# Kernel tuning notes

Hardware: AMD Instinct MI355X
Metric: run time of the kernel (lower is better)

## Reference

```python
import jax, jax.numpy as jnp
import numpy as np

ADMP = 8  # admp_channel -> K = ADMP*ADMP keypoints


def setup_inputs() -> dict:
    key = jax.random.key(0)
    kA, kB = jax.random.split(key)
    B, C, H, W = 8, 512, 96, 96
    feature_A = jax.random.normal(kA, (B, C, H, W), dtype=jnp.float32)
    feature_B = jax.random.normal(kB, (B, C, H, W), dtype=jnp.float32)
    return {"feature_A": feature_A, "feature_B": feature_B}


def _keypoint_rowcol(feature_A):
    # featureSelect: sum over channels, AdaptiveMaxPool2d(ADMP) with return_indices.
    # H,W divisible by ADMP so adaptive pool == uniform non-overlapping pooling.
    B, C, H, W = feature_A.shape
    ph, pw = H // ADMP, W // ADMP
    resp = feature_A.sum(axis=1)  # [B,H,W]
    r = resp.reshape(B, ADMP, ph, ADMP, pw).transpose(0, 1, 3, 2, 4)
    r = r.reshape(B, ADMP * ADMP, ph * pw)
    loc = jnp.argmax(r, axis=-1)  # first-max, matches torch  [B,K]
    kk = jnp.arange(ADMP * ADMP)
    gi, gj = kk // ADMP, kk % ADMP
    row_A = gi[None, :] * ph + loc // pw  # [B,K]
    col_A = gj[None, :] * pw + loc % pw
    return row_A, col_A


def reference(feature_A, feature_B):
    B, C, H, W = feature_A.shape
    K = ADMP * ADMP
    row_A, col_A = _keypoint_rowcol(feature_A)
    flat_A = row_A * W + col_A  # [B,K]

    # gather descriptors: [B,K,C]
    fa = feature_A.reshape(B, C, H * W)
    desc = jnp.take_along_axis(fa, flat_A[:, None, :], axis=2).transpose(0, 2, 1)

    # squared L2 distance map via ||b||^2 - 2 a.b + ||a||^2 : [B,K,HW]
    fb = feature_B.reshape(B, C, H * W)
    fb_sq = jnp.sum(fb * fb, axis=1)            # [B,HW]
    d_sq = jnp.sum(desc * desc, axis=-1)        # [B,K]
    cross = jnp.einsum('bkc,bcn->bkn', desc, fb)  # [B,K,HW]
    dist = fb_sq[:, None, :] - 2.0 * cross + d_sq[:, :, None]

    min_idx = jnp.argmin(dist, axis=-1)  # [B,K]
    row_B = min_idx // W
    col_B = min_idx % W
    drow = -(row_B - row_A)
    dcol = -(col_B - col_A)
    off = jnp.stack([drow, dcol], axis=-1)  # [B,K,2] int

    # getTranslationalOffsetByMode: most frequent (drow,dcol) pair per batch
    eq = jnp.all(off[:, :, None, :] == off[:, None, :, :], axis=-1)  # [B,K,K]
    counts = eq.sum(axis=-1)  # [B,K]
    best = jnp.argmax(counts, axis=-1)  # first occurrence on ties, matches dict order
    out = jnp.take_along_axis(off, best[:, None, None], axis=1)[:, 0, :]  # [B,2]
    return out
```

## Files before the change

### kernel.cpp

```cpp
#include <hip/hip_runtime.h>
#include <hip/hip_bf16.h>
#include <math.h>

typedef _Float16 half8 __attribute__((ext_vector_type(8)));
typedef __fp16 fp16x2 __attribute__((ext_vector_type(2)));
typedef float f32x4 __attribute__((ext_vector_type(4)));
typedef unsigned short u16x4 __attribute__((ext_vector_type(4)));
typedef unsigned short u16x8 __attribute__((ext_vector_type(8)));
typedef unsigned long long u64;

#define B_   8
#define C_   512
#define H_   96
#define W_   96
#define HW   9216
#define K_   64
#define PH   12
#define PW   12
#define NT   96
#define CCH  32
#define NBLK 96

#define OFF_PARTIAL 0u
#define OFF_DESCH   2359296u
#define OFF_DESCL   2883584u
#define OFF_ROWA    3407872u
#define OFF_COLA    3409920u
#define OFF_SLOTS   3411968u

#define FBT_HI 0
#define FBT_LO 3072
#define DSC_HI 6144
#define DSC_LO 8704
#define BUFHW  11264

__global__ __launch_bounds__(256) void k_partial(const float* __restrict__ A,
                                                 float* __restrict__ part,
                                                 u64* __restrict__ slots) {
    if (blockIdx.x == 0 && blockIdx.y == 0) {
        slots[threadIdx.x] = ~0ull;
        slots[threadIdx.x + 256] = ~0ull;
    }
    int bxs = (blockIdx.x & 7) * 9 + (blockIdx.x >> 3);
    int idx4 = bxs * 256 + threadIdx.x;
    int chunk = blockIdx.y;
    int b = idx4 / (HW / 4), hw4 = idx4 - b * (HW / 4);
    const float* p = A + ((size_t)(b * C_ + chunk * 64)) * HW + hw4 * 4;
    float4 s = make_float4(0.f, 0.f, 0.f, 0.f);
#pragma unroll
    for (int i = 0; i < 64; ++i) {
        float4 v = *(const float4*)&p[(size_t)i * HW];
        s.x += v.x; s.y += v.y; s.z += v.z; s.w += v.w;
    }
    *(float4*)&part[chunk * (B_ * HW) + b * HW + hw4 * 4] = s;
}

__global__ void k_selgather(const float* __restrict__ part, const float* __restrict__ A,
                            int* __restrict__ rowA, int* __restrict__ colA,
                            _Float16* __restrict__ descH, _Float16* __restrict__ descL) {
    int k = blockIdx.x, b = blockIdx.y, lane = threadIdx.x;
    int gi = k >> 3, gj = k & 7;
    float bv = -1e30f; int bp = 1 << 20;
    for (int p = lane; p < PH * PW; p += 64) {
        int lr = p / PW, lc = p - lr * PW;
        int hw = (gi * PH + lr) * W_ + gj * PW + lc;
        float v = 0.f;
#pragma unroll
        for (int ch = 0; ch < 8; ++ch) v += part[ch * (B_ * HW) + b * HW + hw];
        if (v > bv || (v == bv && p < bp)) { bv = v; bp = p; }
    }
    for (int m = 1; m < 64; m <<= 1) {
        float ov = __shfl_xor(bv, m);
        int   op = __shfl_xor(bp, m);
        if (ov > bv || (ov == bv && op < bp)) { bv = ov; bp = op; }
    }
    int lr = bp / PW, lc = bp - lr * PW;
    int r = gi * PH + lr, c = gj * PW + lc;
    int flat = r * W_ + c;
    if (lane == 0) { rowA[b * K_ + k] = r; colA[b * K_ + k] = c; }
#pragma unroll
    for (int i = 0; i < 8; ++i) {
        int cc = i * 64 + lane;
        float v = A[((size_t)(b * C_ + cc)) * HW + flat];
        _Float16 h = (_Float16)v;
        _Float16 lo = (_Float16)((v - (float)h) * 2048.f);
        size_t o = ((size_t)(b * K_ + k)) * C_ + cc;
        descH[o] = h; descL[o] = lo;
    }
}

__global__ __launch_bounds__(256, 3) void k_main(const float* __restrict__ FB,
                                                 const _Float16* __restrict__ descH,
                                                 const _Float16* __restrict__ descL,
                                                 u64* __restrict__ slots) {
    __shared__ __attribute__((aligned(16))) unsigned short smem_us[2 * BUFHW];
    int b = blockIdx.y;
    int bxs = (blockIdx.x & 7) * 12 + (blockIdx.x >> 3);
    int nb = bxs * NT;
    int tid = threadIdx.x;
    int l = tid & 63;
    int w = tid >> 6;
    const size_t baseB = (size_t)b * C_ * HW + nb;

    const int so = tid % 12;
    const int scb = tid / 12;
    const int st_nt = so >> 1, st_nn0 = (so & 1) * 8;
    const int dk = tid >> 2, dco = tid & 3;

    f32x4 accH[6], accX[6];
#pragma unroll
    for (int nt = 0; nt < 6; ++nt) {
        accH[nt] = (f32x4){0.f, 0.f, 0.f, 0.f};
        accX[nt] = (f32x4){0.f, 0.f, 0.f, 0.f};
    }
    float sq[8];
#pragma unroll
    for (int j = 0; j < 8; ++j) sq[j] = 0.f;

    float4 Ar0a, Ar0b, Ar1a, Ar1b; u16x8 ArdH, ArdL;
    float4 Br0a, Br0b, Br1a, Br1b; u16x8 BrdH, BrdL;

#define LOADALL(S, c0)                                                        \
    do {                                                                      \
        if (tid < 192) {                                                      \
            const float* p0 = &FB[baseB + (size_t)((c0) + scb) * HW + so * 8];      \
            const float* p1 = &FB[baseB + (size_t)((c0) + scb + 16) * HW + so * 8]; \
            S##r0a = *(const float4*)p0; S##r0b = *(const float4*)(p0 + 4);   \
            S##r1a = *(const float4*)p1; S##r1b = *(const float4*)(p1 + 4);   \
        }                                                                     \
        size_t o = ((size_t)(b * K_) + dk) * C_ + (c0) + dco * 8;             \
        S##rdH = *(const u16x8*)&descH[o];                                    \
        S##rdL = *(const u16x8*)&descL[o];                                    \
    } while (0)

#define CVT8(va, vb, hofs)                                                    \
    do {                                                                      \
        union { fp16x2 p[4]; half8 h; } hh, ll;                               \
        float vv[8] = {va.x, va.y, va.z, va.w, vb.x, vb.y, vb.z, vb.w};       \
        _Pragma("unroll")                                                     \
        for (int j = 0; j < 4; ++j) {                                         \
            float a = vv[2 * j], bq = vv[2 * j + 1];                          \
            fp16x2 hp = __builtin_amdgcn_cvt_pkrtz(a, bq);                    \
            float ha = (float)hp[0], hb = (float)hp[1];                       \
            fp16x2 lp = __builtin_amdgcn_cvt_pkrtz((a - ha) * 2048.f,         \
                                                   (bq - hb) * 2048.f);       \
            hh.p[j] = hp; ll.p[j] = lp;                                       \
            sq[2 * j]     = fmaf(a, a, sq[2 * j]);                            \
            sq[2 * j + 1] = fmaf(bq, bq, sq[2 * j + 1]);                      \
        }                                                                     \
        *(half8*)&smem_us[(hofs)] = hh.h;                                     \
        *(half8*)&smem_us[(hofs) + FBT_LO] = ll.h;                            \
    } while (0)

#define WRITEALL(S, bufhw)                                                    \
    do {                                                                      \
        if (tid < 192) {                                                      \
            int c = scb;                                                      \
            int off0 = (bufhw) + FBT_HI + st_nt * 512 + ((c >> 2) & 1) * 256  \
                       + (c >> 3) * 64 + (c & 3) * 16 + st_nn0;               \
            CVT8(S##r0a, S##r0b, off0);                                       \
            c = scb + 16;                                                     \
            int off1 = (bufhw) + FBT_HI + st_nt * 512 + ((c >> 2) & 1) * 256  \
                       + (c >> 3) * 64 + (c & 3) * 16 + st_nn0;               \
            CVT8(S##r1a, S##r1b, off1);                                       \
        }                                                                     \
        *(u16x8*)&smem_us[(bufhw) + DSC_HI + dk * 40 + dco * 8] = S##rdH;     \
        *(u16x8*)&smem_us[(bufhw) + DSC_LO + dk * 40 + dco * 8] = S##rdL;     \
    } while (0)

    const unsigned lds0 = (unsigned)(size_t)&smem_us[0];

#define TRQ(d0, d1, d2, d3, addr)                                             \
    asm volatile("ds_read_b64_tr_b16 %0, %1"             : "=v"(d0) : "v"(addr)); \
    asm volatile("ds_read_b64_tr_b16 %0, %1 offset:512"  : "=v"(d1) : "v"(addr)); \
    asm volatile("ds_read_b64_tr_b16 %0, %1 offset:6144" : "=v"(d2) : "v"(addr)); \
    asm volatile("ds_read_b64_tr_b16 %0, %1 offset:6656" : "=v"(d3) : "v"(addr));

#define WAIT8 asm volatile("s_waitcnt lgkmcnt(8)" ::: "memory");              \
              __builtin_amdgcn_sched_barrier(0);
#define WAIT4 asm volatile("s_waitcnt lgkmcnt(4)" ::: "memory");              \
              __builtin_amdgcn_sched_barrier(0);
#define WAIT0 asm volatile("s_waitcnt lgkmcnt(0)" ::: "memory");              \
              __builtin_amdgcn_sched_barrier(0);

#define MFMA3(nt, h0_, h1_, l0_, l1_)                                         \
    do {                                                                      \
        union { u16x4 q[2]; half8 h; } bh, bl;                                \
        bh.q[0] = h0_; bh.q[1] = h1_; bl.q[0] = l0_; bl.q[1] = l1_;           \
        accH[nt] = __builtin_amdgcn_mfma_f32_16x16x32_f16(aHu.h, bh.h, accH[nt], 0, 0, 0); \
        accX[nt] = __builtin_amdgcn_mfma_f32_16x16x32_f16(aHu.h, bl.h, accX[nt], 0, 0, 0); \
        accX[nt] = __builtin_amdgcn_mfma_f32_16x16x32_f16(aLu.h, bh.h, accX[nt], 0, 0, 0); \
    } while (0)

#define COMPUTE(cur)                                                          \
    do {                                                                      \
        union { u16x8 u; half8 h; } aHu, aLu;                                 \
        const unsigned abase = lds0 +                                         \
            (unsigned)((cur) + DSC_HI + (w * 16 + (l & 15)) * 40 + (l >> 4) * 8) * 2u; \
        __builtin_amdgcn_s_setprio(1);                                        \
        asm volatile("ds_read_b128 %0, %1"             : "=v"(aHu.u) : "v"(abase)); \
        asm volatile("ds_read_b128 %0, %1 offset:5120" : "=v"(aLu.u) : "v"(abase)); \
        const unsigned trb = lds0 + (unsigned)(cur) * 2u + (unsigned)l * 8u;  \
        u16x4 xh0, xh1, xl0, xl1, yh0, yh1, yl0, yl1, zh0, zh1, zl0, zl1;     \
        TRQ(xh0, xh1, xl0, xl1, trb);                                         \
        TRQ(yh0, yh1, yl0, yl1, trb + 1024u);                                 \
        TRQ(zh0, zh1, zl0, zl1, trb + 2048u);                                 \
        WAIT8;                                                                \
        MFMA3(0, xh0, xh1, xl0, xl1);                                         \
        TRQ(xh0, xh1, xl0, xl1, trb + 3072u);                                 \
        WAIT8;                                                                \
        MFMA3(1, yh0, yh1, yl0, yl1);                                         \
        TRQ(yh0, yh1, yl0, yl1, trb + 4096u);                                 \
        WAIT8;                                                                \
        MFMA3(2, zh0, zh1, zl0, zl1);                                         \
        TRQ(zh0, zh1, zl0, zl1, trb + 5120u);                                 \
        WAIT8;                                                                \
        MFMA3(3, xh0, xh1, xl0, xl1);                                         \
        WAIT4;                                                                \
        MFMA3(4, yh0, yh1, yl0, yl1);                                         \
        WAIT0;                                                                \
        MFMA3(5, zh0, zh1, zl0, zl1);                                         \
        __builtin_amdgcn_s_setprio(0);                                        \
    } while (0)

    LOADALL(A, 0);
    WRITEALL(A, 0);
    LOADALL(B, CCH);
    __syncthreads();

#pragma unroll 1
    for (int tp = 0; tp < 8; ++tp) {
        const int t0 = 2 * tp, t1 = 2 * tp + 1;
        if (t0 + 2 < 16) LOADALL(A, (t0 + 2) * CCH);
        COMPUTE(0);
        if (t0 + 1 < 16) WRITEALL(B, BUFHW);
        __syncthreads();
        if (t1 + 2 < 16) LOADALL(B, (t1 + 2) * CCH);
        COMPUTE(BUFHW);
        if (t1 + 1 < 16) WRITEALL(A, 0);
        __syncthreads();
    }

    float* fscr = (float*)&smem_us[0];
    if (tid < 192) {
        *(float4*)&fscr[scb * 96 + so * 8]     = make_float4(sq[0], sq[1], sq[2], sq[3]);
        *(float4*)&fscr[scb * 96 + so * 8 + 4] = make_float4(sq[4], sq[5], sq[6], sq[7]);
    }
    __syncthreads();
    if (tid < 96) {
        float s = 0.f;
#pragma unroll
        for (int g = 0; g < 16; ++g) s += fscr[g * 96 + tid];
        fscr[1536 + tid] = s;
    }
    __syncthreads();

    const float inv2048 = 1.f / 2048.f;
#pragma unroll
    for (int r = 0; r < 4; ++r) {
        float bv = 1e30f; int bn = 1 << 28;
#pragma unroll
        for (int nt = 0; nt < 6; ++nt) {
            float cross = accH[nt][r] + accX[nt][r] * inv2048;
            float d = fscr[1536 + nt * 16 + (l & 15)] - 2.f * cross;
            int n = nb + nt * 16 + (l & 15);
            if (d < bv) { bv = d; bn = n; }
        }
#pragma unroll
        for (int m = 1; m < 16; m <<= 1) {
            float ov = __shfl_xor(bv, m);
            int   on = __shfl_xor(bn, m);
            if (ov < bv || (ov == bv && on < bn)) { bv = ov; bn = on; }
        }
        if ((l & 15) == 0) {
            int k = w * 16 + (l >> 4) * 4 + r;
            unsigned bits = __float_as_uint(bv);
            unsigned key = (bits & 0x80000000u) ? ~bits : (bits | 0x80000000u);
            u64 packed = ((u64)key << 32) | (unsigned)bn;
            atomicMin(&slots[b * K_ + k], packed);
        }
    }
#undef LOADALL
#undef CVT8
#undef WRITEALL
#undef TRQ
#undef WAIT8
#undef WAIT4
#undef WAIT0
#undef MFMA3
#undef COMPUTE
}

__global__ void k_redmode(const u64* __restrict__ slots,
                          const int* __restrict__ rowA, const int* __restrict__ colA,
                          int* __restrict__ out) {
    __shared__ int r_s[64], c_s[64];
    int b = blockIdx.x, k = threadIdx.x;
    u64 s = slots[b * K_ + k];
    int bn = (int)(unsigned)(s & 0xFFFFFFFFull);
    int rB = bn / W_, cB = bn - rB * W_;
    r_s[k] = rowA[b * K_ + k] - rB;
    c_s[k] = colA[b * K_ + k] - cB;
    __syncthreads();
    int mr = r_s[k], mc = c_s[k], cnt = 0;
#pragma unroll
    for (int j = 0; j < 64; ++j) cnt += (r_s[j] == mr && c_s[j] == mc) ? 1 : 0;
    int bk = k, bc = cnt;
    for (int m = 1; m < 64; m <<= 1) {
        int oc = __shfl_xor(bc, m);
        int ok = __shfl_xor(bk, m);
        if (oc > bc || (oc == bc && ok < bk)) { bc = oc; bk = ok; }
    }
    if (k == 0) { out[b * 2] = r_s[bk]; out[b * 2 + 1] = c_s[bk]; }
}

extern "C" void kernel_launch(void* const* d_in, const int* in_sizes, int n_in,
                              void* d_out, int out_size, void* d_ws, size_t ws_size,
                              hipStream_t stream) {
    const float* A  = (const float*)d_in[0];
    const float* FB = (const float*)d_in[1];
    char* ws = (char*)d_ws;
    float*     part  = (float*)(ws + OFF_PARTIAL);
    _Float16*  descH = (_Float16*)(ws + OFF_DESCH);
    _Float16*  descL = (_Float16*)(ws + OFF_DESCL);
    int*       rowA  = (int*)(ws + OFF_ROWA);
    int*       colA  = (int*)(ws + OFF_COLA);
    u64*       slots = (u64*)(ws + OFF_SLOTS);
    int*       out   = (int*)d_out;

    k_partial<<<dim3((B_ * HW) / 1024, 8), 256, 0, stream>>>(A, part, slots);
    k_selgather<<<dim3(K_, B_), 64, 0, stream>>>(part, A, rowA, colA, descH, descL);
    k_main<<<dim3(NBLK, B_), 256, 0, stream>>>(FB, descH, descL, slots);
    k_redmode<<<dim3(B_), 64, 0, stream>>>(slots, rowA, colA, out);
}
```

Measured before the change: 82.77 us.

## Load descriptor MFMA operands directly into registers, drop LDS staging

Descriptor hi/lo fragments now go straight from global memory into the per-lane MFMA A-operand registers and are double-buffered in registers, so they no longer pass through shared memory. This removes the LDS writes and ds_read_b128 for descriptors and shrinks the per-buffer LDS footprint. The FB prefetch is cut to one register set and issued just before compute, one stage ahead instead of two, which shortens how much global latency it can hide. The descriptor global loads are also less coalesced, since each lane now fetches its own k-row fragment.

```diff
diff --git a/kernel.cpp b/kernel.cpp
--- a/kernel.cpp
+++ b/kernel.cpp
@@ -28,11 +28,8 @@
 #define OFF_COLA    3409920u
 #define OFF_SLOTS   3411968u
 
-#define FBT_HI 0
 #define FBT_LO 3072
-#define DSC_HI 6144
-#define DSC_LO 8704
-#define BUFHW  11264
+#define BUFHW  6144
 
 __global__ __launch_bounds__(256) void k_partial(const float* __restrict__ A,
                                                  float* __restrict__ part,
@@ -105,7 +102,7 @@
     const int so = tid % 12;
     const int scb = tid / 12;
     const int st_nt = so >> 1, st_nn0 = (so & 1) * 8;
-    const int dk = tid >> 2, dco = tid & 3;
+    const size_t dbase = ((size_t)(b * K_) + w * 16 + (l & 15)) * C_ + (l >> 4) * 8;
 
     f32x4 accH[6], accX[6];
 #pragma unroll
@@ -117,20 +114,23 @@
 #pragma unroll
     for (int j = 0; j < 8; ++j) sq[j] = 0.f;
 
-    float4 Ar0a, Ar0b, Ar1a, Ar1b; u16x8 ArdH, ArdL;
-    float4 Br0a, Br0b, Br1a, Br1b; u16x8 BrdH, BrdL;
-
-#define LOADALL(S, c0)                                                        \
+    float4 r0a, r0b, r1a, r1b;
+    u16x8 AdH, AdL, BdH, BdL;
+
+#define LOADFB(c0)                                                            \
     do {                                                                      \
         if (tid < 192) {                                                      \
             const float* p0 = &FB[baseB + (size_t)((c0) + scb) * HW + so * 8];      \
             const float* p1 = &FB[baseB + (size_t)((c0) + scb + 16) * HW + so * 8]; \
-            S##r0a = *(const float4*)p0; S##r0b = *(const float4*)(p0 + 4);   \
-            S##r1a = *(const float4*)p1; S##r1b = *(const float4*)(p1 + 4);   \
+            r0a = *(const float4*)p0; r0b = *(const float4*)(p0 + 4);         \
+            r1a = *(const float4*)p1; r1b = *(const float4*)(p1 + 4);         \
         }                                                                     \
-        size_t o = ((size_t)(b * K_) + dk) * C_ + (c0) + dco * 8;             \
-        S##rdH = *(const u16x8*)&descH[o];                                    \
-        S##rdL = *(const u16x8*)&descL[o];                                    \
+    } while (0)
+
+#define LOADDESC(S, c0)                                                       \
+    do {                                                                      \
+        S##dH = *(const u16x8*)&descH[dbase + (c0)];                          \
+        S##dL = *(const u16x8*)&descL[dbase + (c0)];                          \
     } while (0)
 
 #define CVT8(va, vb, hofs)                                                    \
@@ -152,20 +152,18 @@
         *(half8*)&smem_us[(hofs) + FBT_LO] = ll.h;                            \
     } while (0)
 
-#define WRITEALL(S, bufhw)                                                    \
+#define WRITEFB(bufhw)                                                        \
     do {                                                                      \
         if (tid < 192) {                                                      \
             int c = scb;                                                      \
-            int off0 = (bufhw) + FBT_HI + st_nt * 512 + ((c >> 2) & 1) * 256  \
+            int off0 = (bufhw) + st_nt * 512 + ((c >> 2) & 1) * 256           \
                        + (c >> 3) * 64 + (c & 3) * 16 + st_nn0;               \
-            CVT8(S##r0a, S##r0b, off0);                                       \
+            CVT8(r0a, r0b, off0);                                             \
             c = scb + 16;                                                     \
-            int off1 = (bufhw) + FBT_HI + st_nt * 512 + ((c >> 2) & 1) * 256  \
+            int off1 = (bufhw) + st_nt * 512 + ((c >> 2) & 1) * 256           \
                        + (c >> 3) * 64 + (c & 3) * 16 + st_nn0;               \
-            CVT8(S##r1a, S##r1b, off1);                                       \
+            CVT8(r1a, r1b, off1);                                             \
         }                                                                     \
-        *(u16x8*)&smem_us[(bufhw) + DSC_HI + dk * 40 + dco * 8] = S##rdH;     \
-        *(u16x8*)&smem_us[(bufhw) + DSC_LO + dk * 40 + dco * 8] = S##rdL;     \
     } while (0)
 
     const unsigned lds0 = (unsigned)(size_t)&smem_us[0];
@@ -192,14 +190,11 @@
         accX[nt] = __builtin_amdgcn_mfma_f32_16x16x32_f16(aLu.h, bh.h, accX[nt], 0, 0, 0); \
     } while (0)
 
-#define COMPUTE(cur)                                                          \
+#define COMPUTE(cur, S)                                                       \
     do {                                                                      \
         union { u16x8 u; half8 h; } aHu, aLu;                                 \
-        const unsigned abase = lds0 +                                         \
-            (unsigned)((cur) + DSC_HI + (w * 16 + (l & 15)) * 40 + (l >> 4) * 8) * 2u; \
+        aHu.u = S##dH; aLu.u = S##dL;                                         \
         __builtin_amdgcn_s_setprio(1);                                        \
-        asm volatile("ds_read_b128 %0, %1"             : "=v"(aHu.u) : "v"(abase)); \
-        asm volatile("ds_read_b128 %0, %1 offset:5120" : "=v"(aLu.u) : "v"(abase)); \
         const unsigned trb = lds0 + (unsigned)(cur) * 2u + (unsigned)l * 8u;  \
         u16x4 xh0, xh1, xl0, xl1, yh0, yh1, yl0, yl1, zh0, zh1, zl0, zl1;     \
         TRQ(xh0, xh1, xl0, xl1, trb);                                         \
@@ -223,21 +218,24 @@
         __builtin_amdgcn_s_setprio(0);                                        \
     } while (0)
 
-    LOADALL(A, 0);
-    WRITEALL(A, 0);
-    LOADALL(B, CCH);
+    LOADFB(0);
+    LOADDESC(A, 0);
+    LOADDESC(B, CCH);
+    WRITEFB(0);
     __syncthreads();
 
 #pragma unroll 1
     for (int tp = 0; tp < 8; ++tp) {
         const int t0 = 2 * tp, t1 = 2 * tp + 1;
-        if (t0 + 2 < 16) LOADALL(A, (t0 + 2) * CCH);
-        COMPUTE(0);
-        if (t0 + 1 < 16) WRITEALL(B, BUFHW);
+        LOADFB((t0 + 1) * CCH);
+        COMPUTE(0, A);
+        if (t0 + 2 < 16) LOADDESC(A, (t0 + 2) * CCH);
+        WRITEFB(BUFHW);
         __syncthreads();
-        if (t1 + 2 < 16) LOADALL(B, (t1 + 2) * CCH);
-        COMPUTE(BUFHW);
-        if (t1 + 1 < 16) WRITEALL(A, 0);
+        if (t1 + 1 < 16) LOADFB((t1 + 1) * CCH);
+        COMPUTE(BUFHW, B);
+        if (t1 + 2 < 16) LOADDESC(B, (t1 + 2) * CCH);
+        if (t1 + 1 < 16) WRITEFB(0);
         __syncthreads();
     }
 
@@ -280,9 +278,10 @@
             atomicMin(&slots[b * K_ + k], packed);
         }
     }
-#undef LOADALL
+#undef LOADFB
+#undef LOADDESC
 #undef CVT8
-#undef WRITEALL
+#undef WRITEFB
 #undef TRQ
 #undef WAIT8
 #undef WAIT4
```

Result: no change. 81.99 us, median of 2 (-0.9%).
